# Optimization experiments

Measured on AMD Instinct MI355X. Metric: run time of the kernel, lower is better.

## Reference

```python
import jax, jax.numpy as jnp
import numpy as np

N = 100000
E = 1600000
F_IN = 128
DIM = 32
NUM_CLASSES = 40
BN_EPS = 1e-5


def setup_inputs() -> dict:
    key = jax.random.key(0)
    ks = jax.random.split(key, 16)
    inp = {}
    inp['x'] = jax.random.normal(ks[0], (N, F_IN), dtype=jnp.float32)
    inp['edge_index'] = jax.random.randint(ks[1], (2, E), 0, N, dtype=jnp.int64)
    s = lambda fan_in: 1.0 / np.sqrt(fan_in)
    # GINConv 1 MLP: Linear(F_IN, DIM) -> ReLU -> Linear(DIM, DIM)
    inp['w1a'] = jax.random.uniform(ks[2], (F_IN, DIM), jnp.float32, -s(F_IN), s(F_IN))
    inp['b1a'] = jnp.zeros((DIM,), jnp.float32)
    inp['w1b'] = jax.random.uniform(ks[3], (DIM, DIM), jnp.float32, -s(DIM), s(DIM))
    inp['b1b'] = jnp.zeros((DIM,), jnp.float32)
    # GINConv 2 MLP: Linear(DIM, DIM) -> ReLU -> Linear(DIM, DIM)
    inp['w2a'] = jax.random.uniform(ks[4], (DIM, DIM), jnp.float32, -s(DIM), s(DIM))
    inp['b2a'] = jnp.zeros((DIM,), jnp.float32)
    inp['w2b'] = jax.random.uniform(ks[5], (DIM, DIM), jnp.float32, -s(DIM), s(DIM))
    inp['b2b'] = jnp.zeros((DIM,), jnp.float32)
    # BatchNorm params (eval mode: running stats)
    inp['bn1_g'] = jnp.ones((DIM,), jnp.float32)
    inp['bn1_b'] = jnp.zeros((DIM,), jnp.float32)
    inp['bn1_m'] = jax.random.normal(ks[6], (DIM,), jnp.float32) * 0.1
    inp['bn1_v'] = jax.random.uniform(ks[7], (DIM,), jnp.float32, 0.5, 1.5)
    inp['bn2_g'] = jnp.ones((DIM,), jnp.float32)
    inp['bn2_b'] = jnp.zeros((DIM,), jnp.float32)
    inp['bn2_m'] = jax.random.normal(ks[8], (DIM,), jnp.float32) * 0.1
    inp['bn2_v'] = jax.random.uniform(ks[9], (DIM,), jnp.float32, 0.5, 1.5)
    # FC heads
    inp['fc1_w'] = jax.random.uniform(ks[10], (DIM, DIM), jnp.float32, -s(DIM), s(DIM))
    inp['fc1_b'] = jnp.zeros((DIM,), jnp.float32)
    inp['fc2_w'] = jax.random.uniform(ks[11], (DIM, NUM_CLASSES), jnp.float32, -s(DIM), s(DIM))
    inp['fc2_b'] = jnp.zeros((NUM_CLASSES,), jnp.float32)
    return inp


def _gin_conv(x, src, dst, wa, ba, wb, bb):
    # sum-aggregate neighbor features (messages flow src -> dst), eps = 0
    agg = jax.ops.segment_sum(x[src], dst, num_segments=N)
    h = agg + x  # (1 + eps) * x + sum_j x_j
    h = jax.nn.relu(h @ wa + ba)
    return h @ wb + bb


def _bn(x, g, b, m, v):
    return (x - m) * (g * jax.lax.rsqrt(v + BN_EPS)) + b


def reference(x, edge_index, w1a, b1a, w1b, b1b, w2a, b2a, w2b, b2b,
              bn1_g, bn1_b, bn1_m, bn1_v, bn2_g, bn2_b, bn2_m, bn2_v,
              fc1_w, fc1_b, fc2_w, fc2_b):
    src, dst = edge_index[0], edge_index[1]
    h = jax.nn.relu(_gin_conv(x, src, dst, w1a, b1a, w1b, b1b))
    h = _bn(h, bn1_g, bn1_b, bn1_m, bn1_v)  # dropout is identity in eval
    h = _gin_conv(h, src, dst, w2a, b2a, w2b, b2b)
    h = _bn(h, bn2_g, bn2_b, bn2_m, bn2_v)
    h = jax.nn.relu(h @ fc1_w + fc1_b)
    logits = h @ fc2_w + fc2_b
    return jax.nn.log_softmax(logits, axis=1)
```

## Files before the change

kernel.cpp:

```cpp
#include <hip/hip_runtime.h>
#include <hip/hip_bf16.h>

static constexpr int N_   = 100000;
static constexpr int E_   = 1600000;
static constexpr int FIN_ = 128;
static constexpr int DIM_ = 32;
static constexpr int NC_  = 40;
static constexpr int NB_BKT = (N_ + 127) / 128;
static constexpr int NCHUNK = 256;
static constexpr int EPC    = E_ / NCHUNK;

__global__ void detect_kernel(const void* __restrict__ edge, int* __restrict__ flag) {
    if (blockIdx.x == 0) {
        const long long* p = (const long long*)edge;
        long long v = p[threadIdx.x & 63];
        bool bad = (v < 0 || v >= (long long)N_);
        unsigned long long m = __ballot(bad);
        if (threadIdx.x == 0) *flag = (m == 0ull) ? 1 : 0;
    }
}

__device__ __forceinline__ int edge_at(const void* e, int is64, long long i) {
    return is64 ? (int)((const long long*)e)[i] : ((const int*)e)[i];
}

__device__ __forceinline__ float bflo(unsigned u) { return __uint_as_float(u << 16); }
__device__ __forceinline__ float bfhi(unsigned u) { return __uint_as_float(u & 0xffff0000u); }

__global__ __launch_bounds__(256) void chist_kernel(const void* __restrict__ edge,
                                                    const int* __restrict__ flag,
                                                    int* __restrict__ ghist) {
    __shared__ int lh[NB_BKT];
    for (int i = threadIdx.x; i < NB_BKT; i += 256) lh[i] = 0;
    __syncthreads();
    int f = *flag;
    int b = blockIdx.x;
    int end = b * EPC + EPC;
    for (int e = b * EPC + threadIdx.x; e < end; e += 256) {
        int d = edge_at(edge, f, (long long)E_ + e);
        atomicAdd(&lh[d >> 7], 1);
    }
    __syncthreads();
    for (int i = threadIdx.x; i < NB_BKT; i += 256) ghist[b * NB_BKT + i] = lh[i];
}

__global__ __launch_bounds__(NCHUNK) void colscan_kernel(const int* __restrict__ ghist,
                                                         int* __restrict__ gcurT,
                                                         int* __restrict__ bcnt) {
    __shared__ int a[NCHUNK];
    int k = blockIdx.x, tid = threadIdx.x;
    int v = ghist[tid * NB_BKT + k];
    a[tid] = v;
    __syncthreads();
    for (int off = 1; off < NCHUNK; off <<= 1) {
        int t = a[tid] + ((tid >= off) ? a[tid - off] : 0);
        __syncthreads();
        a[tid] = t;
        __syncthreads();
    }
    gcurT[k * NCHUNK + tid] = a[tid] - v;
    if (tid == NCHUNK - 1) bcnt[k] = a[tid];
}

__global__ __launch_bounds__(1024) void bscan_kernel(const int* __restrict__ bcnt,
                                                     int* __restrict__ bbase,
                                                     int* __restrict__ offs) {
    __shared__ int a[1024];
    int tid = threadIdx.x;
    int v = (tid < NB_BKT) ? bcnt[tid] : 0;
    a[tid] = v;
    __syncthreads();
    for (int off = 1; off < 1024; off <<= 1) {
        int t = a[tid] + ((tid >= off) ? a[tid - off] : 0);
        __syncthreads();
        a[tid] = t;
        __syncthreads();
    }
    if (tid < NB_BKT) bbase[tid] = a[tid] - v;
    if (tid == NB_BKT - 1) offs[N_] = a[tid];
}

__global__ __launch_bounds__(256) void dscatter_kernel(const void* __restrict__ edge,
                                                       const int* __restrict__ flag,
                                                       const int* __restrict__ bbase,
                                                       const int* __restrict__ gcurT,
                                                       int* __restrict__ packed) {
    __shared__ int cur[NB_BKT];
    int b = blockIdx.x, tid = threadIdx.x;
    for (int k = tid; k < NB_BKT; k += 256) cur[k] = bbase[k] + gcurT[k * NCHUNK + b];
    __syncthreads();
    int f = *flag;
    int end = b * EPC + EPC;
    for (int e = b * EPC + tid; e < end; e += 256) {
        int s = edge_at(edge, f, e);
        int d = edge_at(edge, f, (long long)E_ + e);
        int pos = atomicAdd(&cur[d >> 7], 1);
        packed[pos] = s | ((d & 127) << 17);
    }
}

__global__ __launch_bounds__(256) void bsort_kernel(const int* __restrict__ bcnt,
                                                    const int* __restrict__ bbase,
                                                    const int* __restrict__ packed,
                                                    int* __restrict__ offs,
                                                    int* __restrict__ csr) {
    __shared__ int c[128];
    __shared__ int cur[128];
    int tid = threadIdx.x;
    int b = blockIdx.x;
    int beg = bbase[b], cnt = bcnt[b];
    if (tid < 128) c[tid] = 0;
    __syncthreads();
    for (int i = tid; i < cnt; i += 256)
        atomicAdd(&c[packed[beg + i] >> 17], 1);
    __syncthreads();
    int myv = (tid < 128) ? c[tid] : 0;
    for (int off = 1; off < 128; off <<= 1) {
        int t = 0;
        if (tid < 128) t = c[tid] + ((tid >= off) ? c[tid - off] : 0);
        __syncthreads();
        if (tid < 128) c[tid] = t;
        __syncthreads();
    }
    if (tid < 128) {
        int ex = c[tid] - myv;
        cur[tid] = ex;
        int node = b * 128 + tid;
        if (node < N_) offs[node] = beg + ex;
    }
    __syncthreads();
    for (int i = tid; i < cnt; i += 256) {
        int v = packed[beg + i];
        int p = atomicAdd(&cur[v >> 17], 1);
        csr[beg + p] = v & 0x1FFFF;
    }
}

__global__ __launch_bounds__(256) void proj1_kernel(const float* __restrict__ x,
                                                    const float* __restrict__ w,
                                                    __hip_bfloat16* __restrict__ yh) {
    __shared__ float wsm[FIN_ * DIM_];
    __shared__ float xs[32][FIN_];
    int tid = threadIdx.x;

    const float4* w4 = (const float4*)w;
    float4* ws4 = (float4*)wsm;
    for (int i = tid; i < FIN_ * DIM_ / 4; i += 256) ws4[i] = w4[i];

    int nodeBase = blockIdx.x * 32;
    const float4* x4 = (const float4*)(x + (size_t)nodeBase * FIN_);
    float4* xs4 = (float4*)&xs[0][0];
    for (int i = tid; i < 32 * FIN_ / 4; i += 256) xs4[i] = x4[i];
    __syncthreads();

    int d = tid & 31, ns = tid >> 5;
    for (int rep = 0; rep < 4; ++rep) {
        int node = ns + rep * 8;
        float acc = 0.f;
#pragma unroll 4
        for (int k = 0; k < FIN_; ++k) acc += xs[node][k] * wsm[k * DIM_ + d];
        yh[(size_t)(nodeBase + node) * DIM_ + d] = __float2bfloat16(acc);
    }
}

__device__ __forceinline__ void gather_row(const int* __restrict__ csr,
                                           const char* __restrict__ vb,
                                           int beg, int end, int loff,
                                           float& a0, float& a1, float& a2, float& a3) {
    int i = beg;
    for (; i + 3 < end; i += 4) {
        int s0 = csr[i], s1 = csr[i + 1], s2 = csr[i + 2], s3 = csr[i + 3];
        uint2 u0 = *(const uint2*)(vb + (((size_t)s0) << 6) + loff);
        uint2 u1 = *(const uint2*)(vb + (((size_t)s1) << 6) + loff);
        uint2 u2 = *(const uint2*)(vb + (((size_t)s2) << 6) + loff);
        uint2 u3 = *(const uint2*)(vb + (((size_t)s3) << 6) + loff);
        a0 += (bflo(u0.x) + bflo(u1.x)) + (bflo(u2.x) + bflo(u3.x));
        a1 += (bfhi(u0.x) + bfhi(u1.x)) + (bfhi(u2.x) + bfhi(u3.x));
        a2 += (bflo(u0.y) + bflo(u1.y)) + (bflo(u2.y) + bflo(u3.y));
        a3 += (bfhi(u0.y) + bfhi(u1.y)) + (bfhi(u2.y) + bfhi(u3.y));
    }
    for (; i < end; ++i) {
        int s0 = csr[i];
        uint2 u0 = *(const uint2*)(vb + (((size_t)s0) << 6) + loff);
        a0 += bflo(u0.x); a1 += bfhi(u0.x); a2 += bflo(u0.y); a3 += bfhi(u0.y);
    }
}

__global__ __launch_bounds__(256) void aggmlp1_kernel(const int* __restrict__ offs,
                                                      const int* __restrict__ csr,
                                                      const __hip_bfloat16* __restrict__ yh,
                                                      const float* __restrict__ b1a,
                                                      const float* __restrict__ w1b,
                                                      const float* __restrict__ b1b,
                                                      const float* __restrict__ g1,
                                                      const float* __restrict__ be1,
                                                      const float* __restrict__ m1,
                                                      const float* __restrict__ v1,
                                                      const float* __restrict__ w2a,
                                                      __hip_bfloat16* __restrict__ zh) {
    __shared__ float A[32 * 33];
    __shared__ float B[32 * 33];
    __shared__ float w1s[DIM_ * DIM_];
    __shared__ float w2s[DIM_ * DIM_];
    int tid = threadIdx.x;
    for (int i = tid; i < DIM_ * DIM_; i += 256) { w1s[i] = w1b[i]; w2s[i] = w2a[i]; }

    int nl = tid >> 3, lane = tid & 7;
    int node = blockIdx.x * 32 + nl;
    int beg = offs[node], end = offs[node + 1];
    float a0 = 0.f, a1 = 0.f, a2 = 0.f, a3 = 0.f;
    gather_row(csr, (const char*)yh, beg, end, lane << 3, a0, a1, a2, a3);
    {
        float* p = &A[nl * 33 + lane * 4];
        p[0] = a0; p[1] = a1; p[2] = a2; p[3] = a3;
    }
    __syncthreads();

    int d = tid & 31, ng = tid >> 5;
    size_t gbase = (size_t)blockIdx.x * 32 * DIM_;

#pragma unroll
    for (int r = 0; r < 4; ++r) {
        int n = r * 8 + ng;
        float yv = __bfloat162float(yh[gbase + n * DIM_ + d]);
        A[n * 33 + d] = fmaxf(A[n * 33 + d] + yv + b1a[d], 0.f);
    }
    __syncthreads();

    float sc1 = g1[d] * rsqrtf(v1[d] + 1e-5f);
    float sh1 = be1[d] - m1[d] * sc1;

#pragma unroll
    for (int r = 0; r < 4; ++r) {
        int n = r * 8 + ng;
        float acc = b1b[d];
#pragma unroll
        for (int k = 0; k < DIM_; ++k) acc += A[n * 33 + k] * w1s[k * DIM_ + d];
        B[n * 33 + d] = fmaxf(acc, 0.f) * sc1 + sh1;
    }
    __syncthreads();

#pragma unroll
    for (int r = 0; r < 4; ++r) {
        int n = r * 8 + ng;
        float acc = 0.f;
#pragma unroll
        for (int k = 0; k < DIM_; ++k) acc += B[n * 33 + k] * w2s[k * DIM_ + d];
        zh[gbase + n * DIM_ + d] = __float2bfloat16(acc);
    }
}

__global__ __launch_bounds__(256) void aggmlp2_kernel(const int* __restrict__ offs,
                                                      const int* __restrict__ csr,
                                                      const __hip_bfloat16* __restrict__ zh,
                                                      const float* __restrict__ b2a,
                                                      const float* __restrict__ w2b,
                                                      const float* __restrict__ b2b,
                                                      const float* __restrict__ g2,
                                                      const float* __restrict__ be2,
                                                      const float* __restrict__ m2,
                                                      const float* __restrict__ v2,
                                                      const float* __restrict__ f1w,
                                                      const float* __restrict__ f1b,
                                                      const float* __restrict__ f2w,
                                                      const float* __restrict__ f2b,
                                                      float* __restrict__ out) {
    __shared__ float A[32 * 33];
    __shared__ float BC[DIM_ * NC_];
    __shared__ float wA[DIM_ * DIM_];
    __shared__ float wB[DIM_ * DIM_];
    int tid = threadIdx.x;
    for (int i = tid; i < DIM_ * DIM_; i += 256) { wA[i] = w2b[i]; wB[i] = f1w[i]; }

    int nl = tid >> 3, lane = tid & 7;
    int node = blockIdx.x * 32 + nl;
    int beg = offs[node], end = offs[node + 1];
    float a0 = 0.f, a1 = 0.f, a2 = 0.f, a3 = 0.f;
    gather_row(csr, (const char*)zh, beg, end, lane << 3, a0, a1, a2, a3);
    {
        float* p = &A[nl * 33 + lane * 4];
        p[0] = a0; p[1] = a1; p[2] = a2; p[3] = a3;
    }
    __syncthreads();

    int d = tid & 31, ng = tid >> 5;
    size_t gbase = (size_t)blockIdx.x * 32 * DIM_;

#pragma unroll
    for (int r = 0; r < 4; ++r) {
        int n = r * 8 + ng;
        float zv = __bfloat162float(zh[gbase + n * DIM_ + d]);
        A[n * 33 + d] = fmaxf(A[n * 33 + d] + zv + b2a[d], 0.f);
    }
    __syncthreads();

    float sc2 = g2[d] * rsqrtf(v2[d] + 1e-5f);
    float sh2 = be2[d] - m2[d] * sc2;

#pragma unroll
    for (int r = 0; r < 4; ++r) {
        int n = r * 8 + ng;
        float acc = b2b[d];
#pragma unroll
        for (int k = 0; k < DIM_; ++k) acc += A[n * 33 + k] * wA[k * DIM_ + d];
        BC[n * 33 + d] = acc * sc2 + sh2;
    }
    __syncthreads();

#pragma unroll
    for (int r = 0; r < 4; ++r) {
        int n = r * 8 + ng;
        float acc = f1b[d];
#pragma unroll
        for (int k = 0; k < DIM_; ++k) acc += BC[n * 33 + k] * wB[k * DIM_ + d];
        A[n * 33 + d] = fmaxf(acc, 0.f);
    }
    __syncthreads();
    for (int i = tid; i < DIM_ * NC_; i += 256) BC[i] = f2w[i];
    __syncthreads();

    int c2 = 32 + (d & 7);
#pragma unroll
    for (int r = 0; r < 4; ++r) {
        int n = r * 8 + ng;
        float l0 = f2b[d];
        float l1 = f2b[c2];
#pragma unroll
        for (int k = 0; k < DIM_; ++k) {
            float fv = A[n * 33 + k];
            l0 += fv * BC[k * NC_ + d];
            l1 += fv * BC[k * NC_ + c2];
        }
        float mx = fmaxf(l0, l1);
#pragma unroll
        for (int off = 16; off; off >>= 1) mx = fmaxf(mx, __shfl_xor(mx, off));
        float se = __expf(l0 - mx) + ((d < 8) ? __expf(l1 - mx) : 0.f);
#pragma unroll
        for (int off = 16; off; off >>= 1) se += __shfl_xor(se, off);
        float lse = mx + __logf(se);
        size_t ob = (size_t)(blockIdx.x * 32 + n) * NC_;
        out[ob + d] = l0 - lse;
        if (d < 8) out[ob + 32 + d] = l1 - lse;
    }
}

extern "C" void kernel_launch(void* const* d_in, const int* in_sizes, int n_in,
                              void* d_out, int out_size, void* d_ws, size_t ws_size,
                              hipStream_t stream) {
    const float* x   = (const float*)d_in[0];
    const void*  edg = d_in[1];
    const float* w1a = (const float*)d_in[2];
    const float* b1a = (const float*)d_in[3];
    const float* w1b = (const float*)d_in[4];
    const float* b1b = (const float*)d_in[5];
    const float* w2a = (const float*)d_in[6];
    const float* b2a = (const float*)d_in[7];
    const float* w2b = (const float*)d_in[8];
    const float* b2b = (const float*)d_in[9];
    const float* g1  = (const float*)d_in[10];
    const float* be1 = (const float*)d_in[11];
    const float* m1  = (const float*)d_in[12];
    const float* v1  = (const float*)d_in[13];
    const float* g2  = (const float*)d_in[14];
    const float* be2 = (const float*)d_in[15];
    const float* m2  = (const float*)d_in[16];
    const float* v2  = (const float*)d_in[17];
    const float* f1w = (const float*)d_in[18];
    const float* f1b = (const float*)d_in[19];
    const float* f2w = (const float*)d_in[20];
    const float* f2b = (const float*)d_in[21];
    float* out = (float*)d_out;

    char* ws = (char*)d_ws;
    int* flag   = (int*)ws;
    int* bcnt   = (int*)(ws + 256);
    int* bbase  = (int*)(ws + 3584);
    int* ghist  = (int*)(ws + 6912);
    int* gcurT  = (int*)(ws + 807680);
    int* offs   = (int*)(ws + 1608448);
    int* packed = (int*)(ws + 2008576);
    int* csr    = (int*)(ws + 8408576);
    __hip_bfloat16* yh = (__hip_bfloat16*)(ws + 14808576);
    __hip_bfloat16* zh = (__hip_bfloat16*)(ws + 21208576);

    detect_kernel<<<1, 64, 0, stream>>>(edg, flag);

    chist_kernel<<<NCHUNK, 256, 0, stream>>>(edg, flag, ghist);
    colscan_kernel<<<NB_BKT, NCHUNK, 0, stream>>>(ghist, gcurT, bcnt);
    bscan_kernel<<<1, 1024, 0, stream>>>(bcnt, bbase, offs);
    dscatter_kernel<<<NCHUNK, 256, 0, stream>>>(edg, flag, bbase, gcurT, packed);
    bsort_kernel<<<NB_BKT, 256, 0, stream>>>(bcnt, bbase, packed, offs, csr);

    proj1_kernel<<<N_ / 32, 256, 0, stream>>>(x, w1a, yh);
    aggmlp1_kernel<<<N_ / 32, 256, 0, stream>>>(offs, csr, yh, b1a, w1b, b1b,
                                                g1, be1, m1, v1, w2a, zh);

    aggmlp2_kernel<<<N_ / 32, 256, 0, stream>>>(offs, csr, zh, b2a, w2b, b2b,
                                                g2, be2, m2, v2, f1w, f1b, f2w, f2b, out);
}
```

Before: 329.7 us.

## Fuse setup kernels, merge bucket sort with projection, widen gather to 16B

The standalone detect kernel is removed and each block recomputes the int64 detection flag in shared memory. The block-count scan moves into colscan as a last-block-done pattern with an atomic counter. bsort and proj1 are merged into one launch so the sort and the projection can run concurrently. The aggregation kernels now handle 64 nodes per block with 4 lanes per node loading 16 bytes each. Together these cut launch count and per-edge load instructions, at the cost of a memset, redundant per-block detection, and fewer threads per row during the gather.

```diff
diff --git a/kernel.cpp b/kernel.cpp
--- a/kernel.cpp
+++ b/kernel.cpp
@@ -9,16 +9,7 @@
 static constexpr int NB_BKT = (N_ + 127) / 128;
 static constexpr int NCHUNK = 256;
 static constexpr int EPC    = E_ / NCHUNK;
-
-__global__ void detect_kernel(const void* __restrict__ edge, int* __restrict__ flag) {
-    if (blockIdx.x == 0) {
-        const long long* p = (const long long*)edge;
-        long long v = p[threadIdx.x & 63];
-        bool bad = (v < 0 || v >= (long long)N_);
-        unsigned long long m = __ballot(bad);
-        if (threadIdx.x == 0) *flag = (m == 0ull) ? 1 : 0;
-    }
-}
+static constexpr int PROJ_NB = N_ / 32;
 
 __device__ __forceinline__ int edge_at(const void* e, int is64, long long i) {
     return is64 ? (int)((const long long*)e)[i] : ((const int*)e)[i];
@@ -27,13 +18,24 @@
 __device__ __forceinline__ float bflo(unsigned u) { return __uint_as_float(u << 16); }
 __device__ __forceinline__ float bfhi(unsigned u) { return __uint_as_float(u & 0xffff0000u); }
 
+#define DETECT_FLAG(edge, sflag)                                        \
+    if (threadIdx.x < 64) {                                             \
+        const long long* p_ = (const long long*)(edge);                 \
+        long long v_ = p_[threadIdx.x];                                 \
+        bool bad_ = (v_ < 0 || v_ >= (long long)N_);                    \
+        unsigned long long m_ = __ballot(bad_);                         \
+        if (threadIdx.x == 0) sflag = (m_ == 0ull) ? 1 : 0;             \
+    }                                                                   \
+    __syncthreads();
+
 __global__ __launch_bounds__(256) void chist_kernel(const void* __restrict__ edge,
-                                                    const int* __restrict__ flag,
                                                     int* __restrict__ ghist) {
     __shared__ int lh[NB_BKT];
+    __shared__ int sflag;
+    DETECT_FLAG(edge, sflag)
     for (int i = threadIdx.x; i < NB_BKT; i += 256) lh[i] = 0;
     __syncthreads();
-    int f = *flag;
+    int f = sflag;
     int b = blockIdx.x;
     int end = b * EPC + EPC;
     for (int e = b * EPC + threadIdx.x; e < end; e += 256) {
@@ -44,52 +46,60 @@
     for (int i = threadIdx.x; i < NB_BKT; i += 256) ghist[b * NB_BKT + i] = lh[i];
 }
 
-__global__ __launch_bounds__(NCHUNK) void colscan_kernel(const int* __restrict__ ghist,
-                                                         int* __restrict__ gcurT,
-                                                         int* __restrict__ bcnt) {
-    __shared__ int a[NCHUNK];
+__global__ __launch_bounds__(256) void colscan_kernel(const int* __restrict__ ghist,
+                                                      int* __restrict__ gcurT,
+                                                      int* __restrict__ bcnt,
+                                                      int* __restrict__ bbase,
+                                                      int* __restrict__ offs,
+                                                      int* __restrict__ done) {
+    __shared__ int a[256];
+    __shared__ int lastFlag;
     int k = blockIdx.x, tid = threadIdx.x;
     int v = ghist[tid * NB_BKT + k];
     a[tid] = v;
     __syncthreads();
-    for (int off = 1; off < NCHUNK; off <<= 1) {
+    for (int off = 1; off < 256; off <<= 1) {
         int t = a[tid] + ((tid >= off) ? a[tid - off] : 0);
-        __syncthreads();
-        a[tid] = t;
-        __syncthreads();
+        __syncthreads(); a[tid] = t; __syncthreads();
     }
     gcurT[k * NCHUNK + tid] = a[tid] - v;
-    if (tid == NCHUNK - 1) bcnt[k] = a[tid];
-}
-
-__global__ __launch_bounds__(1024) void bscan_kernel(const int* __restrict__ bcnt,
-                                                     int* __restrict__ bbase,
-                                                     int* __restrict__ offs) {
-    __shared__ int a[1024];
-    int tid = threadIdx.x;
-    int v = (tid < NB_BKT) ? bcnt[tid] : 0;
-    a[tid] = v;
-    __syncthreads();
-    for (int off = 1; off < 1024; off <<= 1) {
-        int t = a[tid] + ((tid >= off) ? a[tid - off] : 0);
-        __syncthreads();
-        a[tid] = t;
-        __syncthreads();
-    }
-    if (tid < NB_BKT) bbase[tid] = a[tid] - v;
-    if (tid == NB_BKT - 1) offs[N_] = a[tid];
+    if (tid == 255) {
+        bcnt[k] = a[255];
+        __threadfence();
+        int old = atomicAdd(done, 1);
+        lastFlag = (old == NB_BKT - 1) ? 1 : 0;
+    }
+    __syncthreads();
+    if (lastFlag) {
+        __threadfence();
+        int b4[4]; int base4 = tid * 4; int s = 0;
+#pragma unroll
+        for (int j = 0; j < 4; ++j) { int i = base4 + j; b4[j] = (i < NB_BKT) ? bcnt[i] : 0; s += b4[j]; }
+        __syncthreads();
+        a[tid] = s;
+        __syncthreads();
+        for (int off = 1; off < 256; off <<= 1) {
+            int t = a[tid] + ((tid >= off) ? a[tid - off] : 0);
+            __syncthreads(); a[tid] = t; __syncthreads();
+        }
+        int g = a[tid] - s;
+#pragma unroll
+        for (int j = 0; j < 4; ++j) { int i = base4 + j; if (i < NB_BKT) bbase[i] = g; g += b4[j]; }
+        if (tid == 255) offs[N_] = a[255];
+    }
 }
 
 __global__ __launch_bounds__(256) void dscatter_kernel(const void* __restrict__ edge,
-                                                       const int* __restrict__ flag,
                                                        const int* __restrict__ bbase,
                                                        const int* __restrict__ gcurT,
                                                        int* __restrict__ packed) {
     __shared__ int cur[NB_BKT];
+    __shared__ int sflag;
+    DETECT_FLAG(edge, sflag)
     int b = blockIdx.x, tid = threadIdx.x;
     for (int k = tid; k < NB_BKT; k += 256) cur[k] = bbase[k] + gcurT[k * NCHUNK + b];
     __syncthreads();
-    int f = *flag;
+    int f = sflag;
     int end = b * EPC + EPC;
     for (int e = b * EPC + tid; e < end; e += 256) {
         int s = edge_at(edge, f, e);
@@ -99,90 +109,96 @@
     }
 }
 
-__global__ __launch_bounds__(256) void bsort_kernel(const int* __restrict__ bcnt,
-                                                    const int* __restrict__ bbase,
-                                                    const int* __restrict__ packed,
-                                                    int* __restrict__ offs,
-                                                    int* __restrict__ csr) {
-    __shared__ int c[128];
-    __shared__ int cur[128];
+__global__ __launch_bounds__(256) void fat_kernel(const int* __restrict__ bcnt,
+                                                  const int* __restrict__ bbase,
+                                                  const int* __restrict__ packed,
+                                                  int* __restrict__ offs,
+                                                  int* __restrict__ csr,
+                                                  const float* __restrict__ x,
+                                                  const float* __restrict__ w,
+                                                  __hip_bfloat16* __restrict__ yh) {
+    __shared__ __align__(16) char smem[32768];
     int tid = threadIdx.x;
-    int b = blockIdx.x;
-    int beg = bbase[b], cnt = bcnt[b];
-    if (tid < 128) c[tid] = 0;
-    __syncthreads();
-    for (int i = tid; i < cnt; i += 256)
-        atomicAdd(&c[packed[beg + i] >> 17], 1);
-    __syncthreads();
-    int myv = (tid < 128) ? c[tid] : 0;
-    for (int off = 1; off < 128; off <<= 1) {
-        int t = 0;
-        if (tid < 128) t = c[tid] + ((tid >= off) ? c[tid - off] : 0);
-        __syncthreads();
-        if (tid < 128) c[tid] = t;
-        __syncthreads();
-    }
-    if (tid < 128) {
-        int ex = c[tid] - myv;
-        cur[tid] = ex;
-        int node = b * 128 + tid;
-        if (node < N_) offs[node] = beg + ex;
-    }
-    __syncthreads();
-    for (int i = tid; i < cnt; i += 256) {
-        int v = packed[beg + i];
-        int p = atomicAdd(&cur[v >> 17], 1);
-        csr[beg + p] = v & 0x1FFFF;
-    }
-}
-
-__global__ __launch_bounds__(256) void proj1_kernel(const float* __restrict__ x,
-                                                    const float* __restrict__ w,
-                                                    __hip_bfloat16* __restrict__ yh) {
-    __shared__ float wsm[FIN_ * DIM_];
-    __shared__ float xs[32][FIN_];
-    int tid = threadIdx.x;
-
-    const float4* w4 = (const float4*)w;
-    float4* ws4 = (float4*)wsm;
-    for (int i = tid; i < FIN_ * DIM_ / 4; i += 256) ws4[i] = w4[i];
-
-    int nodeBase = blockIdx.x * 32;
-    const float4* x4 = (const float4*)(x + (size_t)nodeBase * FIN_);
-    float4* xs4 = (float4*)&xs[0][0];
-    for (int i = tid; i < 32 * FIN_ / 4; i += 256) xs4[i] = x4[i];
-    __syncthreads();
-
-    int d = tid & 31, ns = tid >> 5;
-    for (int rep = 0; rep < 4; ++rep) {
-        int node = ns + rep * 8;
-        float acc = 0.f;
+    if (blockIdx.x < NB_BKT) {
+        int* c   = (int*)smem;
+        int* cur = (int*)smem + 128;
+        int b = blockIdx.x;
+        int beg = bbase[b], cnt = bcnt[b];
+        if (tid < 128) c[tid] = 0;
+        __syncthreads();
+        for (int i = tid; i < cnt; i += 256)
+            atomicAdd(&c[packed[beg + i] >> 17], 1);
+        __syncthreads();
+        int myv = (tid < 128) ? c[tid] : 0;
+        for (int off = 1; off < 128; off <<= 1) {
+            int t = 0;
+            if (tid < 128) t = c[tid] + ((tid >= off) ? c[tid - off] : 0);
+            __syncthreads();
+            if (tid < 128) c[tid] = t;
+            __syncthreads();
+        }
+        if (tid < 128) {
+            int ex = c[tid] - myv;
+            cur[tid] = ex;
+            int node = b * 128 + tid;
+            if (node < N_) offs[node] = beg + ex;
+        }
+        __syncthreads();
+        for (int i = tid; i < cnt; i += 256) {
+            int v = packed[beg + i];
+            int p = atomicAdd(&cur[v >> 17], 1);
+            csr[beg + p] = v & 0x1FFFF;
+        }
+    } else {
+        float* wsm = (float*)smem;
+        float* xs  = (float*)(smem + 16384);
+        const float4* w4 = (const float4*)w;
+        float4* ws4 = (float4*)wsm;
+        for (int i = tid; i < FIN_ * DIM_ / 4; i += 256) ws4[i] = w4[i];
+
+        int nodeBase = (blockIdx.x - NB_BKT) * 32;
+        const float4* x4 = (const float4*)(x + (size_t)nodeBase * FIN_);
+        float4* xs4 = (float4*)xs;
+        for (int i = tid; i < 32 * FIN_ / 4; i += 256) xs4[i] = x4[i];
+        __syncthreads();
+
+        int d = tid & 31, ns = tid >> 5;
+        for (int rep = 0; rep < 4; ++rep) {
+            int node = ns + rep * 8;
+            float acc = 0.f;
 #pragma unroll 4
-        for (int k = 0; k < FIN_; ++k) acc += xs[node][k] * wsm[k * DIM_ + d];
-        yh[(size_t)(nodeBase + node) * DIM_ + d] = __float2bfloat16(acc);
-    }
-}
-
-__device__ __forceinline__ void gather_row(const int* __restrict__ csr,
-                                           const char* __restrict__ vb,
-                                           int beg, int end, int loff,
-                                           float& a0, float& a1, float& a2, float& a3) {
+            for (int k = 0; k < FIN_; ++k) acc += xs[node * FIN_ + k] * wsm[k * DIM_ + d];
+            yh[(size_t)(nodeBase + node) * DIM_ + d] = __float2bfloat16(acc);
+        }
+    }
+}
+
+__device__ __forceinline__ void gather_row4(const int* __restrict__ csr,
+                                            const char* __restrict__ vb,
+                                            int beg, int end, int loff, float* acc) {
     int i = beg;
     for (; i + 3 < end; i += 4) {
         int s0 = csr[i], s1 = csr[i + 1], s2 = csr[i + 2], s3 = csr[i + 3];
-        uint2 u0 = *(const uint2*)(vb + (((size_t)s0) << 6) + loff);
-        uint2 u1 = *(const uint2*)(vb + (((size_t)s1) << 6) + loff);
-        uint2 u2 = *(const uint2*)(vb + (((size_t)s2) << 6) + loff);
-        uint2 u3 = *(const uint2*)(vb + (((size_t)s3) << 6) + loff);
-        a0 += (bflo(u0.x) + bflo(u1.x)) + (bflo(u2.x) + bflo(u3.x));
-        a1 += (bfhi(u0.x) + bfhi(u1.x)) + (bfhi(u2.x) + bfhi(u3.x));
-        a2 += (bflo(u0.y) + bflo(u1.y)) + (bflo(u2.y) + bflo(u3.y));
-        a3 += (bfhi(u0.y) + bfhi(u1.y)) + (bfhi(u2.y) + bfhi(u3.y));
+        uint4 u0 = *(const uint4*)(vb + (((size_t)s0) << 6) + loff);
+        uint4 u1 = *(const uint4*)(vb + (((size_t)s1) << 6) + loff);
+        uint4 u2 = *(const uint4*)(vb + (((size_t)s2) << 6) + loff);
+        uint4 u3 = *(const uint4*)(vb + (((size_t)s3) << 6) + loff);
+        acc[0] += (bflo(u0.x) + bflo(u1.x)) + (bflo(u2.x) + bflo(u3.x));
+        acc[1] += (bfhi(u0.x) + bfhi(u1.x)) + (bfhi(u2.x) + bfhi(u3.x));
+        acc[2] += (bflo(u0.y) + bflo(u1.y)) + (bflo(u2.y) + bflo(u3.y));
+        acc[3] += (bfhi(u0.y) + bfhi(u1.y)) + (bfhi(u2.y) + bfhi(u3.y));
+        acc[4] += (bflo(u0.z) + bflo(u1.z)) + (bflo(u2.z) + bflo(u3.z));
+        acc[5] += (bfhi(u0.z) + bfhi(u1.z)) + (bfhi(u2.z) + bfhi(u3.z));
+        acc[6] += (bflo(u0.w) + bflo(u1.w)) + (bflo(u2.w) + bflo(u3.w));
+        acc[7] += (bfhi(u0.w) + bfhi(u1.w)) + (bfhi(u2.w) + bfhi(u3.w));
     }
     for (; i < end; ++i) {
         int s0 = csr[i];
-        uint2 u0 = *(const uint2*)(vb + (((size_t)s0) << 6) + loff);
-        a0 += bflo(u0.x); a1 += bfhi(u0.x); a2 += bflo(u0.y); a3 += bfhi(u0.y);
+        uint4 u0 = *(const uint4*)(vb + (((size_t)s0) << 6) + loff);
+        acc[0] += bflo(u0.x); acc[1] += bfhi(u0.x);
+        acc[2] += bflo(u0.y); acc[3] += bfhi(u0.y);
+        acc[4] += bflo(u0.z); acc[5] += bfhi(u0.z);
+        acc[6] += bflo(u0.w); acc[7] += bfhi(u0.w);
     }
 }
 
@@ -198,32 +214,36 @@
                                                       const float* __restrict__ v1,
                                                       const float* __restrict__ w2a,
                                                       __hip_bfloat16* __restrict__ zh) {
-    __shared__ float A[32 * 33];
-    __shared__ float B[32 * 33];
+    __shared__ float A[64 * 33];
+    __shared__ float B[64 * 33];
     __shared__ float w1s[DIM_ * DIM_];
     __shared__ float w2s[DIM_ * DIM_];
     int tid = threadIdx.x;
     for (int i = tid; i < DIM_ * DIM_; i += 256) { w1s[i] = w1b[i]; w2s[i] = w2a[i]; }
 
-    int nl = tid >> 3, lane = tid & 7;
-    int node = blockIdx.x * 32 + nl;
-    int beg = offs[node], end = offs[node + 1];
-    float a0 = 0.f, a1 = 0.f, a2 = 0.f, a3 = 0.f;
-    gather_row(csr, (const char*)yh, beg, end, lane << 3, a0, a1, a2, a3);
+    int nl = tid >> 2, lane = tid & 3;
+    int node = blockIdx.x * 64 + nl;
+    int beg = 0, end = 0;
+    if (node < N_) { beg = offs[node]; end = offs[node + 1]; }
+    float acc[8] = {0.f, 0.f, 0.f, 0.f, 0.f, 0.f, 0.f, 0.f};
+    gather_row4(csr, (const char*)yh, beg, end, lane << 4, acc);
     {
-        float* p = &A[nl * 33 + lane * 4];
-        p[0] = a0; p[1] = a1; p[2] = a2; p[3] = a3;
+        float* p = &A[nl * 33 + lane * 8];
+#pragma unroll
+        for (int j = 0; j < 8; ++j) p[j] = acc[j];
     }
     __syncthreads();
 
     int d = tid & 31, ng = tid >> 5;
-    size_t gbase = (size_t)blockIdx.x * 32 * DIM_;
-
-#pragma unroll
-    for (int r = 0; r < 4; ++r) {
-        int n = r * 8 + ng;
-        float yv = __bfloat162float(yh[gbase + n * DIM_ + d]);
-        A[n * 33 + d] = fmaxf(A[n * 33 + d] + yv + b1a[d], 0.f);
+    size_t gbase = (size_t)blockIdx.x * 64 * DIM_;
+
+#pragma unroll
+    for (int r = 0; r < 8; ++r) {
+        int n = r * 8 + ng;
+        if (blockIdx.x * 64 + n < N_) {
+            float yv = __bfloat162float(yh[gbase + n * DIM_ + d]);
+            A[n * 33 + d] = fmaxf(A[n * 33 + d] + yv + b1a[d], 0.f);
+        }
     }
     __syncthreads();
 
@@ -231,22 +251,22 @@
     float sh1 = be1[d] - m1[d] * sc1;
 
 #pragma unroll
-    for (int r = 0; r < 4; ++r) {
-        int n = r * 8 + ng;
-        float acc = b1b[d];
-#pragma unroll
-        for (int k = 0; k < DIM_; ++k) acc += A[n * 33 + k] * w1s[k * DIM_ + d];
-        B[n * 33 + d] = fmaxf(acc, 0.f) * sc1 + sh1;
-    }
-    __syncthreads();
-
-#pragma unroll
-    for (int r = 0; r < 4; ++r) {
-        int n = r * 8 + ng;
-        float acc = 0.f;
-#pragma unroll
-        for (int k = 0; k < DIM_; ++k) acc += B[n * 33 + k] * w2s[k * DIM_ + d];
-        zh[gbase + n * DIM_ + d] = __float2bfloat16(acc);
+    for (int r = 0; r < 8; ++r) {
+        int n = r * 8 + ng;
+        float s = b1b[d];
+#pragma unroll
+        for (int k = 0; k < DIM_; ++k) s += A[n * 33 + k] * w1s[k * DIM_ + d];
+        B[n * 33 + d] = fmaxf(s, 0.f) * sc1 + sh1;
+    }
+    __syncthreads();
+
+#pragma unroll
+    for (int r = 0; r < 8; ++r) {
+        int n = r * 8 + ng;
+        float s = 0.f;
+#pragma unroll
+        for (int k = 0; k < DIM_; ++k) s += B[n * 33 + k] * w2s[k * DIM_ + d];
+        if (blockIdx.x * 64 + n < N_) zh[gbase + n * DIM_ + d] = __float2bfloat16(s);
     }
 }
 
@@ -265,32 +285,36 @@
                                                       const float* __restrict__ f2w,
                                                       const float* __restrict__ f2b,
                                                       float* __restrict__ out) {
-    __shared__ float A[32 * 33];
-    __shared__ float BC[DIM_ * NC_];
+    __shared__ float A[64 * 33];
+    __shared__ float BC[64 * 33];
     __shared__ float wA[DIM_ * DIM_];
     __shared__ float wB[DIM_ * DIM_];
     int tid = threadIdx.x;
     for (int i = tid; i < DIM_ * DIM_; i += 256) { wA[i] = w2b[i]; wB[i] = f1w[i]; }
 
-    int nl = tid >> 3, lane = tid & 7;
-    int node = blockIdx.x * 32 + nl;
-    int beg = offs[node], end = offs[node + 1];
-    float a0 = 0.f, a1 = 0.f, a2 = 0.f, a3 = 0.f;
-    gather_row(csr, (const char*)zh, beg, end, lane << 3, a0, a1, a2, a3);
+    int nl = tid >> 2, lane = tid & 3;
+    int node = blockIdx.x * 64 + nl;
+    int beg = 0, end = 0;
+    if (node < N_) { beg = offs[node]; end = offs[node + 1]; }
+    float acc[8] = {0.f, 0.f, 0.f, 0.f, 0.f, 0.f, 0.f, 0.f};
+    gather_row4(csr, (const char*)zh, beg, end, lane << 4, acc);
     {
-        float* p = &A[nl * 33 + lane * 4];
-        p[0] = a0; p[1] = a1; p[2] = a2; p[3] = a3;
+        float* p = &A[nl * 33 + lane * 8];
+#pragma unroll
+        for (int j = 0; j < 8; ++j) p[j] = acc[j];
     }
     __syncthreads();
 
     int d = tid & 31, ng = tid >> 5;
-    size_t gbase = (size_t)blockIdx.x * 32 * DIM_;
-
-#pragma unroll
-    for (int r = 0; r < 4; ++r) {
-        int n = r * 8 + ng;
-        float zv = __bfloat162float(zh[gbase + n * DIM_ + d]);
-        A[n * 33 + d] = fmaxf(A[n * 33 + d] + zv + b2a[d], 0.f);
+    size_t gbase = (size_t)blockIdx.x * 64 * DIM_;
+
+#pragma unroll
+    for (int r = 0; r < 8; ++r) {
+        int n = r * 8 + ng;
+        if (blockIdx.x * 64 + n < N_) {
+            float zv = __bfloat162float(zh[gbase + n * DIM_ + d]);
+            A[n * 33 + d] = fmaxf(A[n * 33 + d] + zv + b2a[d], 0.f);
+        }
     }
     __syncthreads();
 
@@ -298,22 +322,22 @@
     float sh2 = be2[d] - m2[d] * sc2;
 
 #pragma unroll
-    for (int r = 0; r < 4; ++r) {
-        int n = r * 8 + ng;
-        float acc = b2b[d];
-#pragma unroll
-        for (int k = 0; k < DIM_; ++k) acc += A[n * 33 + k] * wA[k * DIM_ + d];
-        BC[n * 33 + d] = acc * sc2 + sh2;
-    }
-    __syncthreads();
-
-#pragma unroll
-    for (int r = 0; r < 4; ++r) {
-        int n = r * 8 + ng;
-        float acc = f1b[d];
-#pragma unroll
-        for (int k = 0; k < DIM_; ++k) acc += BC[n * 33 + k] * wB[k * DIM_ + d];
-        A[n * 33 + d] = fmaxf(acc, 0.f);
+    for (int r = 0; r < 8; ++r) {
+        int n = r * 8 + ng;
+        float s = b2b[d];
+#pragma unroll
+        for (int k = 0; k < DIM_; ++k) s += A[n * 33 + k] * wA[k * DIM_ + d];
+        BC[n * 33 + d] = s * sc2 + sh2;
+    }
+    __syncthreads();
+
+#pragma unroll
+    for (int r = 0; r < 8; ++r) {
+        int n = r * 8 + ng;
+        float s = f1b[d];
+#pragma unroll
+        for (int k = 0; k < DIM_; ++k) s += BC[n * 33 + k] * wB[k * DIM_ + d];
+        A[n * 33 + d] = fmaxf(s, 0.f);
     }
     __syncthreads();
     for (int i = tid; i < DIM_ * NC_; i += 256) BC[i] = f2w[i];
@@ -321,7 +345,7 @@
 
     int c2 = 32 + (d & 7);
 #pragma unroll
-    for (int r = 0; r < 4; ++r) {
+    for (int r = 0; r < 8; ++r) {
         int n = r * 8 + ng;
         float l0 = f2b[d];
         float l1 = f2b[c2];
@@ -338,9 +362,12 @@
 #pragma unroll
         for (int off = 16; off; off >>= 1) se += __shfl_xor(se, off);
         float lse = mx + __logf(se);
-        size_t ob = (size_t)(blockIdx.x * 32 + n) * NC_;
-        out[ob + d] = l0 - lse;
-        if (d < 8) out[ob + 32 + d] = l1 - lse;
+        int gn = blockIdx.x * 64 + n;
+        if (gn < N_) {
+            size_t ob = (size_t)gn * NC_;
+            out[ob + d] = l0 - lse;
+            if (d < 8) out[ob + 32 + d] = l1 - lse;
+        }
     }
 }
 
@@ -372,7 +399,7 @@
     float* out = (float*)d_out;
 
     char* ws = (char*)d_ws;
-    int* flag   = (int*)ws;
+    int* done   = (int*)ws;
     int* bcnt   = (int*)(ws + 256);
     int* bbase  = (int*)(ws + 3584);
     int* ghist  = (int*)(ws + 6912);
@@ -383,18 +410,18 @@
     __hip_bfloat16* yh = (__hip_bfloat16*)(ws + 14808576);
     __hip_bfloat16* zh = (__hip_bfloat16*)(ws + 21208576);
 
-    detect_kernel<<<1, 64, 0, stream>>>(edg, flag);
-
-    chist_kernel<<<NCHUNK, 256, 0, stream>>>(edg, flag, ghist);
-    colscan_kernel<<<NB_BKT, NCHUNK, 0, stream>>>(ghist, gcurT, bcnt);
-    bscan_kernel<<<1, 1024, 0, stream>>>(bcnt, bbase, offs);
-    dscatter_kernel<<<NCHUNK, 256, 0, stream>>>(edg, flag, bbase, gcurT, packed);
-    bsort_kernel<<<NB_BKT, 256, 0, stream>>>(bcnt, bbase, packed, offs, csr);
-
-    proj1_kernel<<<N_ / 32, 256, 0, stream>>>(x, w1a, yh);
-    aggmlp1_kernel<<<N_ / 32, 256, 0, stream>>>(offs, csr, yh, b1a, w1b, b1b,
-                                                g1, be1, m1, v1, w2a, zh);
-
-    aggmlp2_kernel<<<N_ / 32, 256, 0, stream>>>(offs, csr, zh, b2a, w2b, b2b,
-                                                g2, be2, m2, v2, f1w, f1b, f2w, f2b, out);
-}
+    hipMemsetAsync(done, 0, 4, stream);
+
+    chist_kernel<<<NCHUNK, 256, 0, stream>>>(edg, ghist);
+    colscan_kernel<<<NB_BKT, 256, 0, stream>>>(ghist, gcurT, bcnt, bbase, offs, done);
+    dscatter_kernel<<<NCHUNK, 256, 0, stream>>>(edg, bbase, gcurT, packed);
+    fat_kernel<<<NB_BKT + PROJ_NB, 256, 0, stream>>>(bcnt, bbase, packed, offs, csr,
+                                                     x, w1a, yh);
+
+    aggmlp1_kernel<<<(N_ + 63) / 64, 256, 0, stream>>>(offs, csr, yh, b1a, w1b, b1b,
+                                                       g1, be1, m1, v1, w2a, zh);
+
+    aggmlp2_kernel<<<(N_ + 63) / 64, 256, 0, stream>>>(offs, csr, zh, b2a, w2b, b2b,
+                                                       g2, be2, m2, v2, f1w, f1b,
+                                                       f2w, f2b, out);
+}
```

New measurement: 367.4 us. +11.4%, slower.
